# Optimization experiments

Measured on AMD Instinct MI355X. Metric: run time of the kernel, lower is better.

## Reference

```python
import jax, jax.numpy as jnp
import numpy as np

NUM_HEADS = 32
NUM_KV_GROUPS = 8


def _rope(x, cos, sin):
    # x: [B, H, S, hd]; cos/sin: [S_max, hd]
    S, hd = x.shape[2], x.shape[3]
    x1, x2 = x[..., : hd // 2], x[..., hd // 2 :]
    rotated = jnp.concatenate((-x2, x1), axis=-1)
    c = cos[:S][None, None]
    s = sin[:S][None, None]
    return (x * c + rotated * s).astype(x.dtype)


def setup_inputs() -> dict:
    key = jax.random.key(0)
    ks = jax.random.split(key, 8)
    B, S, D = 2, 2048, 2048
    H, G = NUM_HEADS, NUM_KV_GROUPS
    hd = D // H
    scale = 1.0 / np.sqrt(D)
    return {
        "inputs": jax.random.normal(ks[0], (B, S, D), jnp.float32),
        "mask": jnp.zeros((S, S), jnp.bool_),  # note: original masked_fill is not in-place -> mask unused
        "cos": jax.random.uniform(ks[1], (S, hd), jnp.float32),
        "sin": jax.random.uniform(ks[2], (S, hd), jnp.float32),
        "Wq": jax.random.normal(ks[3], (D, H * hd), jnp.float32) * scale,
        "Wk": jax.random.normal(ks[4], (D, G * hd), jnp.float32) * scale,
        "Wv": jax.random.normal(ks[5], (D, G * hd), jnp.float32) * scale,
        "Wo": jax.random.normal(ks[6], (H * hd, H * hd), jnp.float32) * scale,
    }


def reference(inputs, mask, cos, sin, Wq, Wk, Wv, Wo):
    B, S, D = inputs.shape
    H, G = NUM_HEADS, NUM_KV_GROUPS
    hd = Wq.shape[1] // H
    group_size = H // G

    q = (inputs @ Wq).reshape(B, S, H, hd).transpose(0, 2, 1, 3)  # [B,H,S,hd]
    k = (inputs @ Wk).reshape(B, S, G, hd).transpose(0, 2, 1, 3)  # [B,G,S,hd]
    v = (inputs @ Wv).reshape(B, S, G, hd).transpose(0, 2, 1, 3)

    q = _rope(q, cos, sin)
    k = _rope(k, cos, sin)

    k = jnp.repeat(k, group_size, axis=1)  # [B,H,S,hd]
    v = jnp.repeat(v, group_size, axis=1)

    scores = jnp.einsum("bhqd,bhkd->bhqk", q, k)
    # NOTE: original uses non-inplace masked_fill whose result is discarded,
    # so faithfully NO mask is applied.
    attn = jax.nn.softmax(scores / jnp.sqrt(jnp.float32(hd)).astype(scores.dtype), axis=-1)
    ctx = jnp.einsum("bhqk,bhkd->bhqd", attn, v)
    ctx = ctx.transpose(0, 2, 1, 3).reshape(B, S, H * hd)
    return ctx @ Wo
```

## Files before the change

kernel.cpp:

```cpp
#include <hip/hip_runtime.h>
#include <stdint.h>

typedef __attribute__((ext_vector_type(8))) short short8;
typedef __attribute__((ext_vector_type(4))) short short4v;
typedef __attribute__((ext_vector_type(4))) float float4v;
typedef __attribute__((ext_vector_type(2))) unsigned uint2v;

__device__ __forceinline__ float bf2f(short s) {
  union { unsigned u; float f; } x;
  x.u = ((unsigned)(unsigned short)s) << 16;
  return x.f;
}
__device__ __forceinline__ short f2bf(float f) {
  union { float f; unsigned u; } x;
  x.f = f;
  unsigned r = x.u + 0x7fffu + ((x.u >> 16) & 1u);
  return (short)(r >> 16);
}
__device__ __forceinline__ float fexp2(float x) {
#if __has_builtin(__builtin_amdgcn_exp2f)
  return __builtin_amdgcn_exp2f(x);
#else
  float r;
  asm("v_exp_f32 %0, %1" : "=v"(r) : "v"(x));
  return r;
#endif
}
__device__ __forceinline__ void glds16(const void* g, void* l) {
  __builtin_amdgcn_global_load_lds(
      (const __attribute__((address_space(1))) void*)g,
      (__attribute__((address_space(3))) void*)l, 16, 0, 0);
}
__device__ __forceinline__ void bar() { __builtin_amdgcn_s_barrier(); }

__global__ __launch_bounds__(256) void f32_to_bf16(const float* __restrict__ s,
                                                   short* __restrict__ d) {
  const long i = ((long)blockIdx.x * 256 + threadIdx.x) * 8;
  const float4v a = *(const float4v*)&s[i];
  const float4v b = *(const float4v*)&s[i + 4];
  short8 v;
#pragma unroll
  for (int e = 0; e < 4; ++e) { v[e] = f2bf(a[e]); v[e + 4] = f2bf(b[e]); }
  *(short8*)&d[i] = v;
}

__device__ __forceinline__ void transpose_tile(
    const float* __restrict__ src, short* __restrict__ dst, int R, int C,
    int r0, int c0) {
  __shared__ short t[64 * 72];
  const int tid = threadIdx.x;
#pragma unroll
  for (int r = 0; r < 2; ++r) {
    int c = r * 256 + tid;
    int row = c >> 3, col8 = (c & 7) * 8;
    const float4v a = *(const float4v*)&src[(long)(r0 + row) * C + c0 + col8];
    const float4v b = *(const float4v*)&src[(long)(r0 + row) * C + c0 + col8 + 4];
    short8 v;
#pragma unroll
    for (int e = 0; e < 4; ++e) { v[e] = f2bf(a[e]); v[e + 4] = f2bf(b[e]); }
    *(short8*)&t[row * 72 + col8] = v;
  }
  __syncthreads();
#pragma unroll
  for (int r = 0; r < 2; ++r) {
    int c = r * 256 + tid;
    int orow = c >> 3, ocol8 = (c & 7) * 8;
    short8 w;
#pragma unroll
    for (int e = 0; e < 8; ++e) w[e] = t[(ocol8 + e) * 72 + orow];
    *(short8*)&dst[(long)(c0 + orow) * R + r0 + ocol8] = w;
  }
}

__global__ __launch_bounds__(256) void transpose_f2b(
    const float* __restrict__ src, short* __restrict__ dst, int R, int C) {
  transpose_tile(src, dst, R, C, blockIdx.y * 64, blockIdx.x * 64);
}

__global__ __launch_bounds__(256) void wtrans3(
    const float* __restrict__ Wq, const float* __restrict__ Wk,
    const float* __restrict__ Wv, short* __restrict__ WT) {
  const int z = blockIdx.z;
  const float* src = z == 0 ? Wq : (z == 1 ? Wk : Wv);
  const int C = z == 0 ? 2048 : 512;
  if (blockIdx.x * 64 >= C) return;
  short* dst = WT + (z == 0 ? 0 : (z == 1 ? 2048 * 2048 : 2560 * 2048));
  transpose_tile(src, dst, 2048, C, blockIdx.y * 64, blockIdx.x * 64);
}

__global__ __launch_bounds__(256) void vtrans(const short* __restrict__ Y,
                                              short* __restrict__ Vt,
                                              int ld, int col0) {
  const int bg = blockIdx.y;
  const int b = bg >> 3, gk = bg & 7;
  const int s0 = blockIdx.x * 64;
  __shared__ short t[64 * 72];
  const int tid = threadIdx.x;
#pragma unroll
  for (int r = 0; r < 2; ++r) {
    int c = r * 256 + tid;
    int row = c >> 3, col8 = (c & 7) * 8;
    short8 v = *(const short8*)&Y[(long)(b * 2048 + s0 + row) * ld + col0 + gk * 64 + col8];
    *(short8*)&t[row * 72 + col8] = v;
  }
  __syncthreads();
#pragma unroll
  for (int r = 0; r < 2; ++r) {
    int c = r * 256 + tid;
    int d = c >> 3, s8 = (c & 7) * 8;
    short8 w;
#pragma unroll
    for (int e = 0; e < 8; ++e) w[e] = t[(s8 + e) * 72 + d];
    *(short8*)&Vt[((long)bg * 64 + d) * 2048 + s0 + s8] = w;
  }
}

template <int MODE>
__global__ __launch_bounds__(256) void gemm_bt(
    const short* __restrict__ A, const short* __restrict__ BT,
    float* __restrict__ Cf, short* __restrict__ Qr, short* __restrict__ Kr,
    short* __restrict__ YV, const float* __restrict__ cosp,
    const float* __restrict__ sinp, int M, int N, int K) {
  (void)M;
  __shared__ short As[128 * 32];
  __shared__ short Bs[128 * 32];
  const int tid = threadIdx.x;
  const int wave = tid >> 6, lane = tid & 63;
  const int g = lane >> 4, lr = lane & 15;
  const int wr = wave >> 1, wc = wave & 1;

  const int nbx = gridDim.x;
  const int nwg = nbx * gridDim.y;
  const int bid = blockIdx.y * nbx + blockIdx.x;
  const int nbid = (bid & 7) * (nwg >> 3) + (bid >> 3);
  const int m0 = (nbid / nbx) << 7, n0 = (nbid % nbx) << 7;

  float4v acc[4][4];
#pragma unroll
  for (int i = 0; i < 4; ++i)
#pragma unroll
    for (int j = 0; j < 4; ++j) acc[i][j] = (float4v)0.f;

  for (int kt = 0; kt < K; kt += 32) {
#pragma unroll
    for (int r = 0; r < 2; ++r) {
      const int cb = r * 256 + wave * 64;
      const int c = cb + lane;
      const int row = c >> 2, kc = c & 3;
      glds16(A + (long)(m0 + row) * K + kt + kc * 8, As + cb * 8);
      glds16(BT + (long)(n0 + row) * K + kt + kc * 8, Bs + cb * 8);
    }
    __syncthreads();
    short8 af[4], bfr[4];
#pragma unroll
    for (int i = 0; i < 4; ++i)
      af[i] = *(const short8*)&As[(wr * 64 + i * 16 + lr) * 32 + g * 8];
#pragma unroll
    for (int j = 0; j < 4; ++j)
      bfr[j] = *(const short8*)&Bs[(wc * 64 + j * 16 + lr) * 32 + g * 8];
#pragma unroll
    for (int i = 0; i < 4; ++i)
#pragma unroll
      for (int j = 0; j < 4; ++j)
        acc[i][j] = __builtin_amdgcn_mfma_f32_16x16x32_bf16(af[i], bfr[j], acc[i][j], 0, 0, 0);
    __syncthreads();
  }

  if constexpr (MODE == 1) {
    const int h = (n0 + wc * 64) >> 6;
#pragma unroll
    for (int i = 0; i < 4; ++i)
#pragma unroll
      for (int t = 0; t < 4; ++t) {
        const int r = m0 + wr * 64 + i * 16 + g * 4 + t;
        const int s = r & 2047, bb = r >> 11;
        if (h < 40) {
          const float sc = h < 32 ? 0.18033688011112043f : 1.0f;
          short* base = h < 32
              ? Qr + ((long)(bb * 32 + h) * 2048 + s) * 64
              : Kr + ((long)(bb * 8 + (h - 32)) * 2048 + s) * 64;
          const float* cr = cosp + s * 64;
          const float* sr = sinp + s * 64;
#pragma unroll
          for (int j = 0; j < 2; ++j) {
            const int d = j * 16 + lr;
            const float x1 = acc[i][j][t];
            const float x2 = acc[i][j + 2][t];
            base[d] = f2bf((x1 * cr[d] - x2 * sr[d]) * sc);
            base[d + 32] = f2bf((x2 * cr[d + 32] + x1 * sr[d + 32]) * sc);
          }
        } else {
          short* base = YV + ((long)bb * 2048 + s) * 512 + (h - 40) * 64;
#pragma unroll
          for (int j = 0; j < 4; ++j) base[j * 16 + lr] = f2bf(acc[i][j][t]);
        }
      }
  } else {
#pragma unroll
    for (int i = 0; i < 4; ++i)
#pragma unroll
      for (int j = 0; j < 4; ++j)
#pragma unroll
        for (int t = 0; t < 4; ++t) {
          const int r = m0 + wr * 64 + i * 16 + g * 4 + t;
          const int cc = n0 + wc * 64 + j * 16 + lr;
          Cf[(long)r * N + cc] = acc[i][j][t];
        }
  }
}

__global__ __launch_bounds__(512, 6) void attn_kernel(
    const short* __restrict__ Qr, const short* __restrict__ Kr,
    const short* __restrict__ Vt, short* __restrict__ Ctx) {
  constexpr int S = 2048;
  constexpr int NIT = 32;
  const int bh = blockIdx.y;
  const int b = bh >> 5, h = bh & 31;
  const int gk = h >> 2;
  const int q0 = blockIdx.x << 7;
  const int tid = threadIdx.x;
  const int w = tid >> 6, lane = tid & 63;
  const int g = lane >> 4, lr = lane & 15;
  const int b8 = lr & 7;
  const int qrow = w * 16 + lr;

  __shared__ short Ks[2][64 * 64];
  __shared__ short Vs[2][64 * 64];
  __shared__ short Ps[128 * 64];

  const short* Qb = Qr + (long)(b * 32 + h) * S * 64;
  const short* Kb = Kr + (long)(b * 8 + gk) * S * 64;
  const short* Vb = Vt + (long)(b * 8 + gk) * 64 * S;

  const int ko0 = lr * 64 + ((0 + g) ^ b8) * 8;
  const int ko1 = lr * 64 + ((4 + g) ^ b8) * 8;
  int vo[2], pr[2], pw[4];
#pragma unroll
  for (int ks = 0; ks < 2; ++ks) {
    vo[ks] = lr * 64 + ((ks * 4 + g) ^ b8) * 8;
    pr[ks] = qrow * 64 + ((ks * 4 + g) ^ b8) * 8;
  }
#pragma unroll
  for (int i = 0; i < 4; ++i)
    pw[i] = qrow * 64 + ((2 * i + (g >> 1)) ^ b8) * 8 + (g & 1) * 4;

  const int srow = tid >> 3, sl = tid & 7;
  const long koff = (long)srow * 64 + (sl ^ (srow & 7)) * 8;
  const long voff = (long)srow * S + (sl ^ (srow & 7)) * 8;

  short8 qf[2];
  qf[0] = *(const short8*)&Qb[(long)(q0 + qrow) * 64 + g * 8];
  qf[1] = *(const short8*)&Qb[(long)(q0 + qrow) * 64 + 32 + g * 8];

  const short8 ones = (short8)(short)0x3F80;
  float4v lacc = (float4v)0.f;
  float4v oacc[4];
#pragma unroll
  for (int di = 0; di < 4; ++di) oacc[di] = (float4v)0.f;

  glds16(Kb + koff, &Ks[0][w * 512]);
  glds16(Vb + voff, &Vs[0][w * 512]);

  for (int it = 0; it < NIT; ++it) {
    const int buf = it & 1;
    if (it + 1 < NIT) {
      glds16(Kb + (long)(it + 1) * 64 * 64 + koff, &Ks[buf ^ 1][w * 512]);
      glds16(Vb + (it + 1) * 64 + voff, &Vs[buf ^ 1][w * 512]);
      asm volatile("s_waitcnt vmcnt(2)" ::: "memory");
    } else {
      asm volatile("s_waitcnt vmcnt(0)" ::: "memory");
    }
    __builtin_amdgcn_sched_barrier(0);
    bar();

    float4v sacc[4];
#pragma unroll
    for (int i = 0; i < 4; ++i) sacc[i] = (float4v)0.f;
    __builtin_amdgcn_s_setprio(1);
#pragma unroll
    for (int i = 0; i < 4; ++i) {
      const short8 a0 = *(const short8*)&Ks[buf][ko0 + i * 1024];
      sacc[i] = __builtin_amdgcn_mfma_f32_16x16x32_bf16(a0, qf[0], sacc[i], 0, 0, 0);
    }
#pragma unroll
    for (int i = 0; i < 4; ++i) {
      const short8 a1 = *(const short8*)&Ks[buf][ko1 + i * 1024];
      sacc[i] = __builtin_amdgcn_mfma_f32_16x16x32_bf16(a1, qf[1], sacc[i], 0, 0, 0);
    }
    __builtin_amdgcn_s_setprio(0);

#pragma unroll
    for (int i = 0; i < 4; ++i) {
      union { float f; unsigned u; } a0, a1, a2, a3;
      a0.f = fexp2(sacc[i][0]);
      a1.f = fexp2(sacc[i][1]);
      a2.f = fexp2(sacc[i][2]);
      a3.f = fexp2(sacc[i][3]);
      const unsigned d0 = __builtin_amdgcn_perm(a1.u + 0x8000u, a0.u + 0x8000u, 0x07060302u);
      const unsigned d1 = __builtin_amdgcn_perm(a3.u + 0x8000u, a2.u + 0x8000u, 0x07060302u);
      *(uint2v*)&Ps[pw[i]] = (uint2v){d0, d1};
    }

    __builtin_amdgcn_s_setprio(1);
#pragma unroll
    for (int ks = 0; ks < 2; ++ks) {
      const short8 pf = *(const short8*)&Ps[pr[ks]];
      lacc = __builtin_amdgcn_mfma_f32_16x16x32_bf16(ones, pf, lacc, 0, 0, 0);
#pragma unroll
      for (int di = 0; di < 4; ++di) {
        const short8 vf = *(const short8*)&Vs[buf][vo[ks] + di * 1024];
        oacc[di] = __builtin_amdgcn_mfma_f32_16x16x32_bf16(vf, pf, oacc[di], 0, 0, 0);
      }
    }
    __builtin_amdgcn_s_setprio(0);
    bar();
  }

  const float inv = 1.f / lacc[0];

  const int q = q0 + qrow;
#pragma unroll
  for (int di = 0; di < 4; ++di) {
    short4v o;
#pragma unroll
    for (int t = 0; t < 4; ++t) o[t] = f2bf(oacc[di][t] * inv);
    *(short4v*)&Ctx[(long)(b * S + q) * 2048 + h * 64 + di * 16 + g * 4] = o;
  }
}

extern "C" void kernel_launch(void* const* d_in, const int* in_sizes, int n_in,
                              void* d_out, int out_size, void* d_ws, size_t ws_size,
                              hipStream_t stream) {
  (void)in_sizes; (void)n_in; (void)out_size; (void)ws_size;
  const float* X    = (const float*)d_in[0];
  const float* cosp = (const float*)d_in[2];
  const float* sinp = (const float*)d_in[3];
  const float* Wq   = (const float*)d_in[4];
  const float* Wk   = (const float*)d_in[5];
  const float* Wv   = (const float*)d_in[6];
  const float* Wo   = (const float*)d_in[7];
  float* out = (float*)d_out;
  char* ws = (char*)d_ws;

  short* Xb = (short*)(ws + 0);
  short* WT = (short*)(ws + 16777216);
  short* Y  = (short*)(ws + 29360128);
  short* Qr = (short*)(ws + 46137344);
  short* Kr = (short*)(ws + 62914560);
  short* YV = (short*)(ws + 67108864);
  short* Vt = (short*)(ws + 71303168);

  f32_to_bf16<<<4096, 256, 0, stream>>>(X, Xb);
  wtrans3<<<dim3(32, 32, 3), 256, 0, stream>>>(Wq, Wk, Wv, WT);

  gemm_bt<1><<<dim3(24, 32), 256, 0, stream>>>(
      Xb, WT, nullptr, Qr, Kr, YV, cosp, sinp, 4096, 3072, 2048);

  transpose_f2b<<<dim3(32, 32), 256, 0, stream>>>(Wo, WT, 2048, 2048);

  vtrans<<<dim3(32, 16), 256, 0, stream>>>(YV, Vt, 512, 0);

  attn_kernel<<<dim3(16, 64), 512, 0, stream>>>(Qr, Kr, Vt, Y);

  gemm_bt<2><<<dim3(16, 32), 256, 0, stream>>>(
      Y, WT, out, nullptr, nullptr, nullptr, nullptr, nullptr, 4096, 2048, 2048);
}
```

Before: 370.4 us.

## Double attention query tile, fuse prep kernels, drop GEMM block swizzle

The attention kernel now processes 256 query rows per block (two 128-row halves), so each K tile loaded into LDS and registers is reused for two query groups. This halves the number of attention blocks and the K/V global traffic, but doubles the accumulator registers, so the occupancy hint is lowered from 6 to 4. Separately, the X conversion and the Wq/Wk/Wv transpose kernels are merged into one launch. The XCD-aware block remapping in the GEMM is replaced with plain blockIdx indexing, which may hurt L2 locality.

```diff
diff --git a/kernel.cpp b/kernel.cpp
--- a/kernel.cpp
+++ b/kernel.cpp
@@ -33,17 +33,6 @@
 }
 __device__ __forceinline__ void bar() { __builtin_amdgcn_s_barrier(); }
 
-__global__ __launch_bounds__(256) void f32_to_bf16(const float* __restrict__ s,
-                                                   short* __restrict__ d) {
-  const long i = ((long)blockIdx.x * 256 + threadIdx.x) * 8;
-  const float4v a = *(const float4v*)&s[i];
-  const float4v b = *(const float4v*)&s[i + 4];
-  short8 v;
-#pragma unroll
-  for (int e = 0; e < 4; ++e) { v[e] = f2bf(a[e]); v[e + 4] = f2bf(b[e]); }
-  *(short8*)&d[i] = v;
-}
-
 __device__ __forceinline__ void transpose_tile(
     const float* __restrict__ src, short* __restrict__ dst, int R, int C,
     int r0, int c0) {
@@ -72,20 +61,34 @@
   }
 }
 
+__global__ __launch_bounds__(256) void prep(
+    const float* __restrict__ X, short* __restrict__ Xb,
+    const float* __restrict__ Wq, const float* __restrict__ Wk,
+    const float* __restrict__ Wv, short* __restrict__ WT) {
+  const int id = blockIdx.x;
+  if (id < 4096) {
+    const long i = ((long)id * 256 + threadIdx.x) * 8;
+    const float4v a = *(const float4v*)&X[i];
+    const float4v b = *(const float4v*)&X[i + 4];
+    short8 v;
+#pragma unroll
+    for (int e = 0; e < 4; ++e) { v[e] = f2bf(a[e]); v[e + 4] = f2bf(b[e]); }
+    *(short8*)&Xb[i] = v;
+  } else {
+    const int r = id - 4096;
+    const int z = r >> 10, bx = r & 31, by = (r >> 5) & 31;
+    const float* src = z == 0 ? Wq : (z == 1 ? Wk : Wv);
+    const int C = z == 0 ? 2048 : 512;
+    if (bx * 64 < C) {
+      short* dst = WT + (z == 0 ? 0 : (z == 1 ? 2048 * 2048 : 2560 * 2048));
+      transpose_tile(src, dst, 2048, C, by * 64, bx * 64);
+    }
+  }
+}
+
 __global__ __launch_bounds__(256) void transpose_f2b(
     const float* __restrict__ src, short* __restrict__ dst, int R, int C) {
   transpose_tile(src, dst, R, C, blockIdx.y * 64, blockIdx.x * 64);
-}
-
-__global__ __launch_bounds__(256) void wtrans3(
-    const float* __restrict__ Wq, const float* __restrict__ Wk,
-    const float* __restrict__ Wv, short* __restrict__ WT) {
-  const int z = blockIdx.z;
-  const float* src = z == 0 ? Wq : (z == 1 ? Wk : Wv);
-  const int C = z == 0 ? 2048 : 512;
-  if (blockIdx.x * 64 >= C) return;
-  short* dst = WT + (z == 0 ? 0 : (z == 1 ? 2048 * 2048 : 2560 * 2048));
-  transpose_tile(src, dst, 2048, C, blockIdx.y * 64, blockIdx.x * 64);
 }
 
 __global__ __launch_bounds__(256) void vtrans(const short* __restrict__ Y,
@@ -128,12 +131,7 @@
   const int wave = tid >> 6, lane = tid & 63;
   const int g = lane >> 4, lr = lane & 15;
   const int wr = wave >> 1, wc = wave & 1;
-
-  const int nbx = gridDim.x;
-  const int nwg = nbx * gridDim.y;
-  const int bid = blockIdx.y * nbx + blockIdx.x;
-  const int nbid = (bid & 7) * (nwg >> 3) + (bid >> 3);
-  const int m0 = (nbid / nbx) << 7, n0 = (nbid % nbx) << 7;
+  const int m0 = blockIdx.y << 7, n0 = blockIdx.x << 7;
 
   float4v acc[4][4];
 #pragma unroll
@@ -209,7 +207,7 @@
   }
 }
 
-__global__ __launch_bounds__(512, 6) void attn_kernel(
+__global__ __launch_bounds__(512, 4) void attn_kernel(
     const short* __restrict__ Qr, const short* __restrict__ Kr,
     const short* __restrict__ Vt, short* __restrict__ Ctx) {
   constexpr int S = 2048;
@@ -217,7 +215,7 @@
   const int bh = blockIdx.y;
   const int b = bh >> 5, h = bh & 31;
   const int gk = h >> 2;
-  const int q0 = blockIdx.x << 7;
+  const int q0 = blockIdx.x << 8;
   const int tid = threadIdx.x;
   const int w = tid >> 6, lane = tid & 63;
   const int g = lane >> 4, lr = lane & 15;
@@ -248,15 +246,22 @@
   const long koff = (long)srow * 64 + (sl ^ (srow & 7)) * 8;
   const long voff = (long)srow * S + (sl ^ (srow & 7)) * 8;
 
-  short8 qf[2];
-  qf[0] = *(const short8*)&Qb[(long)(q0 + qrow) * 64 + g * 8];
-  qf[1] = *(const short8*)&Qb[(long)(q0 + qrow) * 64 + 32 + g * 8];
+  short8 qf[2][2];
+#pragma unroll
+  for (int qh = 0; qh < 2; ++qh) {
+    qf[qh][0] = *(const short8*)&Qb[(long)(q0 + qh * 128 + qrow) * 64 + g * 8];
+    qf[qh][1] = *(const short8*)&Qb[(long)(q0 + qh * 128 + qrow) * 64 + 32 + g * 8];
+  }
 
   const short8 ones = (short8)(short)0x3F80;
-  float4v lacc = (float4v)0.f;
-  float4v oacc[4];
-#pragma unroll
-  for (int di = 0; di < 4; ++di) oacc[di] = (float4v)0.f;
+  float4v lacc[2];
+  float4v oacc[2][4];
+#pragma unroll
+  for (int qh = 0; qh < 2; ++qh) {
+    lacc[qh] = (float4v)0.f;
+#pragma unroll
+    for (int di = 0; di < 4; ++di) oacc[qh][di] = (float4v)0.f;
+  }
 
   glds16(Kb + koff, &Ks[0][w * 512]);
   glds16(Vb + voff, &Vs[0][w * 512]);
@@ -273,58 +278,66 @@
     __builtin_amdgcn_sched_barrier(0);
     bar();
 
-    float4v sacc[4];
-#pragma unroll
-    for (int i = 0; i < 4; ++i) sacc[i] = (float4v)0.f;
-    __builtin_amdgcn_s_setprio(1);
+    short8 kf[8];
 #pragma unroll
     for (int i = 0; i < 4; ++i) {
-      const short8 a0 = *(const short8*)&Ks[buf][ko0 + i * 1024];
-      sacc[i] = __builtin_amdgcn_mfma_f32_16x16x32_bf16(a0, qf[0], sacc[i], 0, 0, 0);
-    }
-#pragma unroll
-    for (int i = 0; i < 4; ++i) {
-      const short8 a1 = *(const short8*)&Ks[buf][ko1 + i * 1024];
-      sacc[i] = __builtin_amdgcn_mfma_f32_16x16x32_bf16(a1, qf[1], sacc[i], 0, 0, 0);
-    }
-    __builtin_amdgcn_s_setprio(0);
-
-#pragma unroll
-    for (int i = 0; i < 4; ++i) {
-      union { float f; unsigned u; } a0, a1, a2, a3;
-      a0.f = fexp2(sacc[i][0]);
-      a1.f = fexp2(sacc[i][1]);
-      a2.f = fexp2(sacc[i][2]);
-      a3.f = fexp2(sacc[i][3]);
-      const unsigned d0 = __builtin_amdgcn_perm(a1.u + 0x8000u, a0.u + 0x8000u, 0x07060302u);
-      const unsigned d1 = __builtin_amdgcn_perm(a3.u + 0x8000u, a2.u + 0x8000u, 0x07060302u);
-      *(uint2v*)&Ps[pw[i]] = (uint2v){d0, d1};
-    }
-
-    __builtin_amdgcn_s_setprio(1);
-#pragma unroll
-    for (int ks = 0; ks < 2; ++ks) {
-      const short8 pf = *(const short8*)&Ps[pr[ks]];
-      lacc = __builtin_amdgcn_mfma_f32_16x16x32_bf16(ones, pf, lacc, 0, 0, 0);
-#pragma unroll
-      for (int di = 0; di < 4; ++di) {
-        const short8 vf = *(const short8*)&Vs[buf][vo[ks] + di * 1024];
-        oacc[di] = __builtin_amdgcn_mfma_f32_16x16x32_bf16(vf, pf, oacc[di], 0, 0, 0);
+      kf[i] = *(const short8*)&Ks[buf][ko0 + i * 1024];
+      kf[4 + i] = *(const short8*)&Ks[buf][ko1 + i * 1024];
+    }
+
+#pragma unroll
+    for (int qh = 0; qh < 2; ++qh) {
+      float4v sacc[4];
+#pragma unroll
+      for (int i = 0; i < 4; ++i) sacc[i] = (float4v)0.f;
+      __builtin_amdgcn_s_setprio(1);
+#pragma unroll
+      for (int i = 0; i < 4; ++i)
+        sacc[i] = __builtin_amdgcn_mfma_f32_16x16x32_bf16(kf[i], qf[qh][0], sacc[i], 0, 0, 0);
+#pragma unroll
+      for (int i = 0; i < 4; ++i)
+        sacc[i] = __builtin_amdgcn_mfma_f32_16x16x32_bf16(kf[4 + i], qf[qh][1], sacc[i], 0, 0, 0);
+      __builtin_amdgcn_s_setprio(0);
+
+#pragma unroll
+      for (int i = 0; i < 4; ++i) {
+        union { float f; unsigned u; } a0, a1, a2, a3;
+        a0.f = fexp2(sacc[i][0]);
+        a1.f = fexp2(sacc[i][1]);
+        a2.f = fexp2(sacc[i][2]);
+        a3.f = fexp2(sacc[i][3]);
+        const unsigned d0 = __builtin_amdgcn_perm(a1.u + 0x8000u, a0.u + 0x8000u, 0x07060302u);
+        const unsigned d1 = __builtin_amdgcn_perm(a3.u + 0x8000u, a2.u + 0x8000u, 0x07060302u);
+        *(uint2v*)&Ps[pw[i]] = (uint2v){d0, d1};
       }
-    }
-    __builtin_amdgcn_s_setprio(0);
+
+      __builtin_amdgcn_s_setprio(1);
+#pragma unroll
+      for (int ks = 0; ks < 2; ++ks) {
+        const short8 pf = *(const short8*)&Ps[pr[ks]];
+        lacc[qh] = __builtin_amdgcn_mfma_f32_16x16x32_bf16(ones, pf, lacc[qh], 0, 0, 0);
+#pragma unroll
+        for (int di = 0; di < 4; ++di) {
+          const short8 vf = *(const short8*)&Vs[buf][vo[ks] + di * 1024];
+          oacc[qh][di] = __builtin_amdgcn_mfma_f32_16x16x32_bf16(vf, pf, oacc[qh][di], 0, 0, 0);
+        }
+      }
+      __builtin_amdgcn_s_setprio(0);
+    }
     bar();
   }
 
-  const float inv = 1.f / lacc[0];
-
-  const int q = q0 + qrow;
-#pragma unroll
-  for (int di = 0; di < 4; ++di) {
-    short4v o;
-#pragma unroll
-    for (int t = 0; t < 4; ++t) o[t] = f2bf(oacc[di][t] * inv);
-    *(short4v*)&Ctx[(long)(b * S + q) * 2048 + h * 64 + di * 16 + g * 4] = o;
+#pragma unroll
+  for (int qh = 0; qh < 2; ++qh) {
+    const float inv = 1.f / lacc[qh][0];
+    const int q = q0 + qh * 128 + qrow;
+#pragma unroll
+    for (int di = 0; di < 4; ++di) {
+      short4v o;
+#pragma unroll
+      for (int t = 0; t < 4; ++t) o[t] = f2bf(oacc[qh][di][t] * inv);
+      *(short4v*)&Ctx[(long)(b * S + q) * 2048 + h * 64 + di * 16 + g * 4] = o;
+    }
   }
 }
 
@@ -350,8 +363,7 @@
   short* YV = (short*)(ws + 67108864);
   short* Vt = (short*)(ws + 71303168);
 
-  f32_to_bf16<<<4096, 256, 0, stream>>>(X, Xb);
-  wtrans3<<<dim3(32, 32, 3), 256, 0, stream>>>(Wq, Wk, Wv, WT);
+  prep<<<7168, 256, 0, stream>>>(X, Xb, Wq, Wk, Wv, WT);
 
   gemm_bt<1><<<dim3(24, 32), 256, 0, stream>>>(
       Xb, WT, nullptr, Qr, Kr, YV, cosp, sinp, 4096, 3072, 2048);
@@ -360,7 +372,7 @@
 
   vtrans<<<dim3(32, 16), 256, 0, stream>>>(YV, Vt, 512, 0);
 
-  attn_kernel<<<dim3(16, 64), 512, 0, stream>>>(Qr, Kr, Vt, Y);
+  attn_kernel<<<dim3(8, 64), 512, 0, stream>>>(Qr, Kr, Vt, Y);
 
   gemm_bt<2><<<dim3(16, 32), 256, 0, stream>>>(
       Y, WT, out, nullptr, nullptr, nullptr, nullptr, nullptr, 4096, 2048, 2048);
```

Result: faster. 355.4 us (-4.1%).
